# Optimization experiments

Measured on AMD Instinct MI355X. Metric: run time of the kernel, lower is better.

## Reference

```python
import jax, jax.numpy as jnp
import numpy as np

BITS = 4
GROUPSIZE = 128
IN_FEATURES = 4096
OUT_FEATURES = 4096
GROUPS = IN_FEATURES // GROUPSIZE  # 32
TOKENS = 8192


def setup_inputs() -> dict:
    key = jax.random.key(0)
    k_x, k_s, k_b = jax.random.split(key, 3)
    rng = np.random.default_rng(0)
    # packed 4-bit weights: 8 nibbles per int32 word
    qweight = jnp.asarray(
        rng.integers(-2**31, 2**31, size=(IN_FEATURES // 8, OUT_FEATURES), dtype=np.int64).astype(np.int32)
    )
    qzeros = jnp.asarray(
        rng.integers(-2**31, 2**31, size=(GROUPS, OUT_FEATURES // 8), dtype=np.int64).astype(np.int32)
    )
    scales = jax.random.uniform(k_s, (GROUPS, OUT_FEATURES), dtype=jnp.float32) * 0.02 + 0.001
    g_idx = (jnp.arange(IN_FEATURES, dtype=jnp.int32) // GROUPSIZE).astype(jnp.int32)
    bias = jax.random.normal(k_b, (OUT_FEATURES,), dtype=jnp.float32) * 0.01
    x = jax.random.normal(k_x, (TOKENS, IN_FEATURES), dtype=jnp.float32)
    return {"x": x, "qweight": qweight, "qzeros": qzeros, "scales": scales,
            "g_idx": g_idx, "bias": bias}


def reference(x, qweight, qzeros, scales, g_idx, bias):
    out_features = qweight.shape[1]
    in_features = qweight.shape[0] * 8
    mask = jnp.int32(15)  # 2**bits - 1
    wf = jnp.arange(0, 32, BITS, dtype=jnp.int32)  # [8] nibble shift amounts
    # unpack zero points: [groups, out//8, 8] -> [groups, out]
    zeros = ((qzeros[:, :, None] >> wf[None, None, :]) & mask) + 1
    zeros = zeros.reshape(scales.shape)
    # unpack weights: [in//8, 8, out] -> [in, out]
    weight = (qweight[:, None, :] >> wf[None, :, None]) & mask
    weight = weight.reshape(in_features, out_features)
    # dequantize per group and matmul
    W = scales[g_idx] * (weight - zeros[g_idx]).astype(scales.dtype)
    out = x @ W
    return out + bias
```

## Files before the change

kernel.cpp:

```cpp
#include <hip/hip_runtime.h>
#include <cstdint>
#include <cstddef>

#define IN_F   4096
#define OUT_F  4096
#define NTOK   8192
#define NGRP   32

#define BM 256
#define BN 256
#define BK 64
#define KTILES   (IN_F / BK)
#define LDS_TILE (BM * BK)

typedef __attribute__((ext_vector_type(8))) __bf16 bf16x8;
typedef __attribute__((ext_vector_type(4))) float  floatx4;

__device__ __forceinline__ unsigned short f2bf(float f) {
    unsigned int u = __builtin_bit_cast(unsigned int, f);
    u += 0x7fffu + ((u >> 16) & 1u);
    return (unsigned short)(u >> 16);
}

__device__ __forceinline__ void gload16(const void* g, void* l) {
    __builtin_amdgcn_global_load_lds(
        (const __attribute__((address_space(1))) void*)g,
        (__attribute__((address_space(3))) void*)l,
        16, 0, 0);
}

__global__ void dequant_kernel(const int* __restrict__ qweight,
                               const int* __restrict__ qzeros,
                               const float* __restrict__ scales,
                               const int* __restrict__ g_idx,
                               unsigned short* __restrict__ Wt) {
    __shared__ unsigned short tile[256 * 64];
    const int tk  = blockIdx.x & 63;
    const int tn  = blockIdx.x >> 6;
    const int tid = threadIdx.x;
    const int n   = tn * 256 + tid;

#pragma unroll
    for (int r = 0; r < 8; ++r) {
        const int k8 = tk * 8 + r;
        const int k  = k8 * 8;
        const int g  = g_idx[k];
        const int qw = qweight[(size_t)k8 * OUT_F + n];
        const float s = scales[g * OUT_F + n];
        const int  zw = qzeros[g * (OUT_F / 8) + (n >> 3)];
        const float z = (float)(((zw >> (4 * (n & 7))) & 15) + 1);
        const float sz = s * z;
        union { unsigned short h[8]; uint4 v; } u;
#pragma unroll
        for (int j = 0; j < 8; ++j)
            u.h[j] = f2bf(s * (float)((qw >> (4 * j)) & 15) - sz);
        *(uint4*)(tile + tid * 64 + ((r ^ (tid & 7)) * 8)) = u.v;
    }
    __syncthreads();
#pragma unroll
    for (int i = 0; i < 8; ++i) {
        const int nl = i * 32 + (tid >> 3);
        const int c  = tid & 7;
        const uint4 v = *(const uint4*)(tile + nl * 64 + ((c ^ (nl & 7)) * 8));
        *(uint4*)(Wt + (size_t)(tn * 256 + nl) * IN_F + tk * 64 + c * 8) = v;
    }
}

__global__ void xcast_kernel(const float* __restrict__ x,
                             unsigned short* __restrict__ Xb) {
    const size_t i = ((size_t)blockIdx.x * 256 + threadIdx.x) * 8;
    const float4 a = *(const float4*)(x + i);
    const float4 b = *(const float4*)(x + i + 4);
    union { unsigned short h[8]; uint4 v; } u;
    u.h[0] = f2bf(a.x); u.h[1] = f2bf(a.y); u.h[2] = f2bf(a.z); u.h[3] = f2bf(a.w);
    u.h[4] = f2bf(b.x); u.h[5] = f2bf(b.y); u.h[6] = f2bf(b.z); u.h[7] = f2bf(b.w);
    *(uint4*)(Xb + i) = u.v;
}

#define VMCNT8() asm volatile("s_waitcnt vmcnt(8)" ::: "memory")
#define VMCNT4() asm volatile("s_waitcnt vmcnt(4)" ::: "memory")
#define VMCNT0() asm volatile("s_waitcnt vmcnt(0)" ::: "memory")
#define BARRIER() do { __builtin_amdgcn_s_barrier(); asm volatile("" ::: "memory"); } while (0)

template<int I0, int J0>
__device__ __forceinline__ void quad(floatx4 (&acc)[8][4],
                                     const bf16x8 (&av)[4][2],
                                     const bf16x8 (&bv)[4][2]) {
#pragma unroll
    for (int i4 = 0; i4 < 4; ++i4)
#pragma unroll
        for (int jj = 0; jj < 2; ++jj)
#pragma unroll
            for (int kk = 0; kk < 2; ++kk)
                acc[I0 + i4][J0 + jj] = __builtin_amdgcn_mfma_f32_16x16x32_bf16(
                    av[i4][kk], bv[J0 + jj][kk], acc[I0 + i4][J0 + jj], 0, 0, 0);
}

__global__ __launch_bounds__(512, 2) void gemm_kernel(
        const unsigned short* __restrict__ Xb,
        const unsigned short* __restrict__ Wt,
        const float* __restrict__ bias,
        float* __restrict__ out) {
    __shared__ unsigned short As[2 * LDS_TILE];
    __shared__ unsigned short Bs[2 * LDS_TILE];

    const int tid  = threadIdx.x;
    const int wave = tid >> 6;
    const int lane = tid & 63;
    const int mi   = lane & 15;
    const int kq   = lane >> 4;

    const int bid = blockIdx.x;
    const int swz = (bid & 7) * 64 + (bid >> 3);
    const int m0  = (swz >> 4) * BM;
    const int n0  = (swz & 15) * BN;

    const int wrow = (wave >> 2) * 128;
    const int wcol = (wave & 3) * 64;

    const int lrow   = lane >> 3;
    const int lchunk = ((lane & 7) ^ lrow) * 8;
    const unsigned short* aSrc = Xb + (size_t)(m0 + lrow) * IN_F + lchunk;
    const unsigned short* bSrc = Wt + (size_t)(n0 + lrow) * IN_F + lchunk;

    const int raA = (wave >> 2) * 128 + (wave & 3) * 16;
    const int raB = (wave >> 1) * 64  + (wave & 1) * 16;

    const int aRd = (wrow + mi) * BK;
    const int bRd = (wcol + mi) * BK;
    const int cp0 = ((kq)     ^ (mi & 7)) * 8;
    const int cp1 = ((4 + kq) ^ (mi & 7)) * 8;

    floatx4 acc[8][4];
#pragma unroll
    for (int i = 0; i < 8; ++i)
#pragma unroll
        for (int j = 0; j < 4; ++j)
            acc[i][j] = floatx4{0.f, 0.f, 0.f, 0.f};

    bf16x8 av[4][2], bv[4][2];

    auto stageA = [&](int bufofs, int h, int kt) {
        const int r0 = raA + h * 64;
        gload16(aSrc + (size_t)(r0 + 0) * IN_F + (size_t)kt * BK,
                (void*)(As + bufofs + (r0 + 0) * BK));
        gload16(aSrc + (size_t)(r0 + 8) * IN_F + (size_t)kt * BK,
                (void*)(As + bufofs + (r0 + 8) * BK));
    };
    auto stageB = [&](int bufofs, int h, int kt) {
        const int r0 = raB + h * 32;
        gload16(bSrc + (size_t)(r0 + 0) * IN_F + (size_t)kt * BK,
                (void*)(Bs + bufofs + (r0 + 0) * BK));
        gload16(bSrc + (size_t)(r0 + 8) * IN_F + (size_t)kt * BK,
                (void*)(Bs + bufofs + (r0 + 8) * BK));
    };
    auto stageAll = [&](int bufofs, int kt) {
        stageA(bufofs, 0, kt);
        stageB(bufofs, 0, kt);
        stageB(bufofs, 1, kt);
        stageA(bufofs, 1, kt);
    };
    auto ldah = [&](int bufofs, int ah) {
#pragma unroll
        for (int i4 = 0; i4 < 4; ++i4) {
            av[i4][0] = *(const bf16x8*)(As + bufofs + aRd + (ah * 4 + i4) * (16 * BK) + cp0);
            av[i4][1] = *(const bf16x8*)(As + bufofs + aRd + (ah * 4 + i4) * (16 * BK) + cp1);
        }
    };
    auto ldb01 = [&](int bufofs) {
#pragma unroll
        for (int jj = 0; jj < 2; ++jj) {
            bv[jj][0] = *(const bf16x8*)(Bs + bufofs + bRd + jj * (16 * BK) + cp0);
            bv[jj][1] = *(const bf16x8*)(Bs + bufofs + bRd + jj * (16 * BK) + cp1);
        }
    };
    auto ldb23 = [&](int bufofs) {
#pragma unroll
        for (int jj = 0; jj < 2; ++jj) {
            bv[2 + jj][0] = *(const bf16x8*)(Bs + bufofs + bRd + (2 + jj) * (16 * BK) + cp0);
            bv[2 + jj][1] = *(const bf16x8*)(Bs + bufofs + bRd + (2 + jj) * (16 * BK) + cp1);
        }
    };

    stageAll(0, 0);
    VMCNT4();
    BARRIER();

    for (int kt = 0; kt < KTILES - 1; ++kt) {
        const int bo = (kt & 1) * LDS_TILE;
        const int no = bo ^ LDS_TILE;

        stageAll(no, kt + 1);
        ldah(bo, 0); ldb01(bo);
        BARRIER();
        __builtin_amdgcn_s_setprio(1);
        quad<0, 0>(acc, av, bv);
        __builtin_amdgcn_s_setprio(0);
        VMCNT8();
        BARRIER();

        ldb23(bo);
        BARRIER();
        __builtin_amdgcn_s_setprio(1);
        quad<0, 2>(acc, av, bv);
        __builtin_amdgcn_s_setprio(0);
        BARRIER();

        ldah(bo, 1);
        BARRIER();
        __builtin_amdgcn_s_setprio(1);
        quad<4, 2>(acc, av, bv);
        __builtin_amdgcn_s_setprio(0);
        BARRIER();

        __builtin_amdgcn_s_setprio(1);
        quad<4, 0>(acc, av, bv);
        __builtin_amdgcn_s_setprio(0);
        VMCNT4();
        BARRIER();
    }

    {
        const int bo = ((KTILES - 1) & 1) * LDS_TILE;
        ldah(bo, 0); ldb01(bo);
        BARRIER();
        __builtin_amdgcn_s_setprio(1);
        quad<0, 0>(acc, av, bv);
        __builtin_amdgcn_s_setprio(0);
        VMCNT0();
        BARRIER();

        ldb23(bo);
        BARRIER();
        __builtin_amdgcn_s_setprio(1);
        quad<0, 2>(acc, av, bv);
        __builtin_amdgcn_s_setprio(0);
        BARRIER();

        ldah(bo, 1);
        BARRIER();
        __builtin_amdgcn_s_setprio(1);
        quad<4, 2>(acc, av, bv);
        quad<4, 0>(acc, av, bv);
        __builtin_amdgcn_s_setprio(0);
    }

    const int mq = kq;
#pragma unroll
    for (int j = 0; j < 4; ++j) {
        const int col = n0 + wcol + j * 16 + mi;
        const float bb = bias[col];
#pragma unroll
        for (int i = 0; i < 8; ++i) {
#pragma unroll
            for (int r = 0; r < 4; ++r) {
                const int row = m0 + wrow + i * 16 + mq * 4 + r;
                out[(size_t)row * OUT_F + col] = acc[i][j][r] + bb;
            }
        }
    }
}

extern "C" void kernel_launch(void* const* d_in, const int* in_sizes, int n_in,
                              void* d_out, int out_size, void* d_ws, size_t ws_size,
                              hipStream_t stream) {
    const float* x       = (const float*)d_in[0];
    const int*   qweight = (const int*)d_in[1];
    const int*   qzeros  = (const int*)d_in[2];
    const float* scales  = (const float*)d_in[3];
    const int*   g_idx   = (const int*)d_in[4];
    const float* bias    = (const float*)d_in[5];
    float*       out     = (float*)d_out;

    unsigned short* Wt = (unsigned short*)d_ws;
    unsigned short* Xb = Wt + (size_t)OUT_F * IN_F;

    dequant_kernel<<<64 * 16, 256, 0, stream>>>(qweight, qzeros, scales, g_idx, Wt);
    xcast_kernel<<<((size_t)NTOK * IN_F / 8) / 256, 256, 0, stream>>>(x, Xb);

    gemm_kernel<<<dim3((NTOK / BM) * (OUT_F / BN)), 512, 0, stream>>>(Xb, Wt, bias, out);
}
```

Baseline: 554.5 us.

## Simplify GEMM main loop to one full-drain barrier per k-tile

Replaces the four-phase ping-pong schedule, which used several barriers, partial vmcnt waits and setprio toggles per k-tile, with a single loop. Each iteration prefetches the next tile, runs all MFMA quads, then waits with vmcnt(0) and one barrier. The peeled last iteration is folded in behind conditionals. This removes barrier overhead, but it loses the fine-grained overlap between global loads and MFMA and the wave-priority interleaving, and the full drain exposes load latency.

Result: faster. 539.6 us (-2.7%).

```diff
diff --git a/kernel.cpp b/kernel.cpp
--- a/kernel.cpp
+++ b/kernel.cpp
@@ -77,10 +77,10 @@
     *(uint4*)(Xb + i) = u.v;
 }
 
-#define VMCNT8() asm volatile("s_waitcnt vmcnt(8)" ::: "memory")
-#define VMCNT4() asm volatile("s_waitcnt vmcnt(4)" ::: "memory")
 #define VMCNT0() asm volatile("s_waitcnt vmcnt(0)" ::: "memory")
-#define BARRIER() do { __builtin_amdgcn_s_barrier(); asm volatile("" ::: "memory"); } while (0)
+#define BAR() do { asm volatile("" ::: "memory"); \
+                   __builtin_amdgcn_s_barrier();  \
+                   asm volatile("" ::: "memory"); } while (0)
 
 template<int I0, int J0>
 __device__ __forceinline__ void quad(floatx4 (&acc)[8][4],
@@ -183,66 +183,28 @@
     };
 
     stageAll(0, 0);
-    VMCNT4();
-    BARRIER();
-
-    for (int kt = 0; kt < KTILES - 1; ++kt) {
+    VMCNT0();
+    BAR();
+
+    for (int kt = 0; kt < KTILES; ++kt) {
         const int bo = (kt & 1) * LDS_TILE;
         const int no = bo ^ LDS_TILE;
 
-        stageAll(no, kt + 1);
+        if (kt < KTILES - 1)
+            stageAll(no, kt + 1);
+
         ldah(bo, 0); ldb01(bo);
-        BARRIER();
-        __builtin_amdgcn_s_setprio(1);
         quad<0, 0>(acc, av, bv);
-        __builtin_amdgcn_s_setprio(0);
-        VMCNT8();
-        BARRIER();
-
         ldb23(bo);
-        BARRIER();
-        __builtin_amdgcn_s_setprio(1);
         quad<0, 2>(acc, av, bv);
-        __builtin_amdgcn_s_setprio(0);
-        BARRIER();
-
         ldah(bo, 1);
-        BARRIER();
-        __builtin_amdgcn_s_setprio(1);
-        quad<4, 2>(acc, av, bv);
-        __builtin_amdgcn_s_setprio(0);
-        BARRIER();
-
-        __builtin_amdgcn_s_setprio(1);
-        quad<4, 0>(acc, av, bv);
-        __builtin_amdgcn_s_setprio(0);
-        VMCNT4();
-        BARRIER();
-    }
-
-    {
-        const int bo = ((KTILES - 1) & 1) * LDS_TILE;
-        ldah(bo, 0); ldb01(bo);
-        BARRIER();
-        __builtin_amdgcn_s_setprio(1);
-        quad<0, 0>(acc, av, bv);
-        __builtin_amdgcn_s_setprio(0);
-        VMCNT0();
-        BARRIER();
-
-        ldb23(bo);
-        BARRIER();
-        __builtin_amdgcn_s_setprio(1);
-        quad<0, 2>(acc, av, bv);
-        __builtin_amdgcn_s_setprio(0);
-        BARRIER();
-
-        ldah(bo, 1);
-        BARRIER();
-        __builtin_amdgcn_s_setprio(1);
         quad<4, 2>(acc, av, bv);
         quad<4, 0>(acc, av, bv);
-        __builtin_amdgcn_s_setprio(0);
+
+        if (kt < KTILES - 1) {
+            VMCNT0();
+            BAR();
+        }
     }
 
     const int mq = kq;
```
